# Optimization experiments

Hardware: AMD Instinct MI355X
Metric: run time of the kernel (lower is better)

## Reference

```python
import jax, jax.numpy as jnp
import numpy as np

B, S, D = 4, 2048, 1024
NH, NKV = 16, 4
HD = D // NH  # 64


def _rope(x, freqs):
    # x: [B, H, S, HD], freqs: [B, S, HD//2]
    cos = jnp.concatenate([jnp.cos(freqs), jnp.cos(freqs)], axis=-1)[:, None]  # [B,1,S,HD]
    sin = jnp.concatenate([jnp.sin(freqs), jnp.sin(freqs)], axis=-1)[:, None]
    x1, x2 = x[..., : HD // 2], x[..., HD // 2:]
    rot = jnp.concatenate([-x2, x1], axis=-1)
    return x * cos + rot * sin


def setup_inputs() -> dict:
    key = jax.random.key(0)
    ks = jax.random.split(key, 9)
    return {
        "hidden_states": jax.random.normal(ks[0], (B, S, D), jnp.float32),
        "rotary_pos_emb": jax.random.normal(ks[1], (B, S, HD // 2), jnp.float32),
        "Wq": jax.random.normal(ks[2], (D, NH * HD), jnp.float32) * 0.02,
        "bq": jax.random.normal(ks[3], (NH * HD,), jnp.float32) * 0.02,
        "Wk": jax.random.normal(ks[4], (D, NKV * HD), jnp.float32) * 0.02,
        "bk": jax.random.normal(ks[5], (NKV * HD,), jnp.float32) * 0.02,
        "Wv": jax.random.normal(ks[6], (D, NKV * HD), jnp.float32) * 0.02,
        "bv": jax.random.normal(ks[7], (NKV * HD,), jnp.float32) * 0.02,
        "Wo": jax.random.normal(ks[8], (NH * HD, D), jnp.float32) * 0.02,
    }


def reference(hidden_states, rotary_pos_emb, Wq, bq, Wk, bk, Wv, bv, Wo):
    b, s, _ = hidden_states.shape
    # projections -> [B, H, S, HD]
    q = (hidden_states @ Wq + bq).reshape(b, s, NH, HD).transpose(0, 2, 1, 3)
    k = (hidden_states @ Wk + bk).reshape(b, s, NKV, HD).transpose(0, 2, 1, 3)
    v = (hidden_states @ Wv + bv).reshape(b, s, NKV, HD).transpose(0, 2, 1, 3)
    q = _rope(q, rotary_pos_emb)
    k = _rope(k, rotary_pos_emb)
    groups = NH // NKV
    k = jnp.repeat(k, groups, axis=1)  # [B, NH, S, HD]
    v = jnp.repeat(v, groups, axis=1)
    scaling = HD ** -0.5
    scores = jnp.einsum("bhqd,bhkd->bhqk", q, k) * scaling
    probs = jax.nn.softmax(scores.astype(jnp.float32), axis=-1).astype(q.dtype)
    out = jnp.einsum("bhqk,bhkd->bhqd", probs, v)
    out = out.transpose(0, 2, 1, 3).reshape(b, s, NH * HD)
    return out @ Wo
```

## Files before the change

### kernel.cpp

```cpp
#include <hip/hip_runtime.h>
#include <hip/hip_bf16.h>

#define BB 4
#define SS 2048
#define DD 1024
#define NH 16
#define NKV 4
#define HD 64
#define MROWS (BB*SS)
#define NQKV (NH*HD + 2*NKV*HD)
#define KOFF (NH*HD)

typedef short v8s __attribute__((ext_vector_type(8)));
typedef short v4s __attribute__((ext_vector_type(4)));
typedef float v4f __attribute__((ext_vector_type(4)));
typedef unsigned short u16;
typedef unsigned int u32;

__device__ __forceinline__ float bf2f(u16 u){
  union { float f; u32 i; } x; x.i = ((u32)u) << 16; return x.f;
}
__device__ __forceinline__ u16 f2bf(float f){
  union { __hip_bfloat16 h; u16 u; } x; x.h = __float2bfloat16(f); return x.u;
}
__device__ __forceinline__ u32 cvtpk(float lo, float hi){
  u32 r;
  asm("v_cvt_pk_bf16_f32 %0, %1, %2" : "=v"(r) : "v"(lo), "v"(hi));
  return r;
}
__device__ __forceinline__ void gl_lds16(const u16* g, u16* l){
  __builtin_amdgcn_global_load_lds(
      (const __attribute__((address_space(1))) u32*)g,
      (__attribute__((address_space(3))) u32*)l, 16, 0, 0);
}


__global__ void prep_fused(const float* __restrict__ Wq, const float* __restrict__ Wk,
                           const float* __restrict__ Wv, const float* __restrict__ bq,
                           const float* __restrict__ bk, const float* __restrict__ bv,
                           const float* __restrict__ Wo, const float* __restrict__ fr,
                           u16* __restrict__ Bqkv, float* __restrict__ bias,
                           u16* __restrict__ WoT, float2* __restrict__ trig){
  int bid = blockIdx.x;
  if (bid < 6144) {
    int idx = bid*256 + threadIdx.x;
    int n = idx >> 10, k = idx & 1023;
    float v;
    if (n < 1024)      v = Wq[k*1024 + n];
    else if (n < 1280) v = Wk[k*256 + (n-1024)];
    else               v = Wv[k*256 + (n-1280)];
    Bqkv[idx] = f2bf(v);
    if (k == 0) bias[n] = (n < 1024) ? bq[n] : (n < 1280 ? bk[n-1024] : bv[n-1280]);
  } else if (bid < 6144 + 4096) {
    int idx = (bid - 6144)*256 + threadIdx.x;
    int n = idx >> 10, k = idx & 1023;
    WoT[idx] = f2bf(Wo[k*1024 + n]);
  } else {
    int i = (bid - 10240)*256 + threadIdx.x;
    float f = fr[i];
    float sn, cs; __sincosf(f, &sn, &cs);
    trig[i] = make_float2(cs, sn);
  }
}

__global__ void rope_k(u16* __restrict__ QKV, const float* __restrict__ fr){
  int idx = blockIdx.x*256 + threadIdx.x;
  int d  = idx & 31;
  int hh = (idx >> 5) & 3;
  long row = idx >> 7;
  int col = KOFF + hh*HD + d;
  u16* p = QKV + row*NQKV;
  float x1 = bf2f(p[col]);
  float x2 = bf2f(p[col+32]);
  float f = fr[row*32 + d];
  float sn, cs; __sincosf(f, &sn, &cs);
  p[col]    = f2bf(x1*cs - x2*sn);
  p[col+32] = f2bf(x2*cs + x1*sn);
}


template<bool BIAS, typename IT, typename OT>
__global__ __launch_bounds__(256) void gemm_bt(
    const IT* __restrict__ A, const u16* __restrict__ Bt,
    const float* __restrict__ bias, OT* __restrict__ C,
    int K, int ldc)
{
  __shared__ u16 As[128*32];
  __shared__ u16 Bs[128*32];
  const int tid = threadIdx.x;
  const int wid = tid >> 6, lane = tid & 63;
  const int g = lane >> 4, c = lane & 15;
  const long brow = (long)blockIdx.y * 128;
  const long bcol = (long)blockIdx.x * 128;
  const int wr = (wid >> 1) * 64, wc = (wid & 1) * 64;
  const int srow = tid >> 2;
  const int scol = (tid & 3) * 8;
  const IT*  ga = &A [(brow + srow)*K + scol];
  const u16* gb = &Bt[(bcol + srow)*K + scol];
  u16* la  = &As[(wid*64)*8];
  u16* lb  = &Bs[(wid*64)*8];
  u16* lwa = &As[srow*32 + scol];
  v4f acc[4][4] = {};
  for (int kt = 0; kt < K; kt += 32) {
    __syncthreads();
    gl_lds16(gb + kt,        lb);
    gl_lds16(gb + 64*K + kt, lb + 256*8);
    if constexpr (sizeof(IT) == 4) {
      float4 a0 = *reinterpret_cast<const float4*>(ga + kt);
      float4 a1 = *reinterpret_cast<const float4*>(ga + kt + 4);
      float4 a2 = *reinterpret_cast<const float4*>(ga + (long)64*K + kt);
      float4 a3 = *reinterpret_cast<const float4*>(ga + (long)64*K + kt + 4);
      union { v8s v; u32 w[4]; } p0, p1;
      p0.w[0] = cvtpk(a0.x, a0.y); p0.w[1] = cvtpk(a0.z, a0.w);
      p0.w[2] = cvtpk(a1.x, a1.y); p0.w[3] = cvtpk(a1.z, a1.w);
      p1.w[0] = cvtpk(a2.x, a2.y); p1.w[1] = cvtpk(a2.z, a2.w);
      p1.w[2] = cvtpk(a3.x, a3.y); p1.w[3] = cvtpk(a3.z, a3.w);
      *reinterpret_cast<v8s*>(lwa)          = p0.v;
      *reinterpret_cast<v8s*>(lwa + 64*32)  = p1.v;
    } else {
      gl_lds16((const u16*)ga + kt,        la);
      gl_lds16((const u16*)ga + 64*K + kt, la + 256*8);
    }
    __syncthreads();
    v8s af[4], bf[4];
    #pragma unroll
    for (int m=0;m<4;m++) af[m] = *reinterpret_cast<const v8s*>(&As[(wr + m*16 + c)*32 + g*8]);
    #pragma unroll
    for (int n=0;n<4;n++) bf[n] = *reinterpret_cast<const v8s*>(&Bs[(wc + n*16 + c)*32 + g*8]);
    __builtin_amdgcn_s_setprio(1);
    #pragma unroll
    for (int m=0;m<4;m++)
      #pragma unroll
      for (int n=0;n<4;n++)
        acc[m][n] = __builtin_amdgcn_mfma_f32_16x16x32_bf16(af[m], bf[n], acc[m][n], 0,0,0);
    __builtin_amdgcn_s_setprio(0);
  }
  #pragma unroll
  for (int m=0;m<4;m++)
    #pragma unroll
    for (int n=0;n<4;n++) {
      int col = (int)bcol + wc + n*16 + c;
      float badd = BIAS ? bias[col] : 0.0f;
      #pragma unroll
      for (int r2=0;r2<4;r2++){
        long row = brow + wr + m*16 + g*4 + r2;
        float v = acc[m][n][r2] + badd;
        if constexpr (sizeof(OT)==2) C[row*ldc + col] = (OT)f2bf(v);
        else                         C[row*ldc + col] = (OT)v;
      }
    }
}


__global__ __launch_bounds__(512) void attn_k(const u16* __restrict__ QKV,
                                              const float2* __restrict__ trig,
                                              u16* __restrict__ Out){
  __shared__ u16 Ks[4][64][72];
  __shared__ u16 Vs[4][64][72];
  const int tid = threadIdx.x;
  const int wid = tid >> 6, lane = tid & 63;
  const int g = lane >> 4, c = lane & 15;
  const int qt = blockIdx.x & 7;
  const int bh = blockIdx.x >> 3;
  const int b = bh >> 4, h = bh & 15;
  const int kvh = h >> 2;
  const u16* Qb = QKV + (long)b*SS*NQKV + h*HD;
  const u16* Kb = QKV + (long)b*SS*NQKV + KOFF + kvh*HD;
  const u16* Vb = Kb + NKV*HD;

  const float SCL = 0.125f * 1.44269504088896f;
  v8s qf[2][2];
  #pragma unroll
  for (int qn=0;qn<2;qn++){
    int lrow = qt*256 + wid*32 + qn*16 + c;
    v8s q0 = *reinterpret_cast<const v8s*>(&Qb[(long)lrow*NQKV + g*8]);
    v8s q1 = *reinterpret_cast<const v8s*>(&Qb[(long)lrow*NQKV + 32 + g*8]);
    const float2* tp = trig + ((long)b*SS + lrow)*32 + g*8;
    union { v8s v; u32 w[4]; } a0, a1;
    #pragma unroll
    for (int wi=0;wi<4;wi++){
      float2 ta = tp[2*wi], tb = tp[2*wi+1];
      float x1a = bf2f((u16)q0[2*wi]),   x2a = bf2f((u16)q1[2*wi]);
      float x1b = bf2f((u16)q0[2*wi+1]), x2b = bf2f((u16)q1[2*wi+1]);
      float r0a = (x1a*ta.x - x2a*ta.y) * SCL;
      float r1a = (x2a*ta.x + x1a*ta.y) * SCL;
      float r0b = (x1b*tb.x - x2b*tb.y) * SCL;
      float r1b = (x2b*tb.x + x1b*tb.y) * SCL;
      a0.w[wi] = cvtpk(r0a, r0b);
      a1.w[wi] = cvtpk(r1a, r1b);
    }
    qf[qn][0] = a0.v; qf[qn][1] = a1.v;
  }

  v8s onesf;
  {
    short ov = (c==0) ? (short)0x3F80 : (short)0;
    #pragma unroll
    for (int j=0;j<8;j++) onesf[j] = ov;
  }

  const v4f vzero = {0.f, 0.f, 0.f, 0.f};
  v4f o[2][5] = {};

  const int krow = tid >> 3;
  const int kcol = (tid & 7) * 8;
  const int key0 = 2*(tid >> 4);
  const int dg4  = (tid & 15) * 4;
  const int slot0 = 32*(key0>>5) + 8*((key0>>2)&3) + 4*((key0>>4)&1) + (key0&3);
  int vofs[4];
  #pragma unroll
  for (int j=0;j<4;j++){
    int d = dg4 + j;
    int idx = (((slot0>>3) ^ (d>>3)) << 3) | (slot0 & 7);
    vofs[j] = d*72 + idx;
  }
  u16* VsF = &Vs[0][0][0];

  const u16* kp  = Kb + (long)krow*NQKV + kcol;
  const u16* vp0 = Vb + (long)key0*NQKV + dg4;
  const u16* vp1 = vp0 + NQKV;

  v8s kregA, kregB;
  union { v4s v; u32 w[2]; } vrA0, vrA1, vrB0, vrB1;

  auto write_tile = [&](int q, const v8s& kr,
                        const u32* wA, const u32* wB){
    *reinterpret_cast<v8s*>(&Ks[q][krow][kcol]) = kr;
    const int bofs = q * (64*72);
    #pragma unroll
    for (int j=0;j<4;j++){
      u32 pkd = __builtin_amdgcn_perm(wB[j>>1], wA[j>>1],
                                      (j&1) ? 0x07060302u : 0x05040100u);
      *reinterpret_cast<u32*>(&VsF[bofs + vofs[j]]) = pkd;
    }
  };

  auto tile_body = [&](int buf){
    v8s kf0[4], kf1[4];
    #pragma unroll
    for (int km=0;km<4;km++){
      kf0[km] = *reinterpret_cast<const v8s*>(&Ks[buf][km*16 + c][g*8]);
      kf1[km] = *reinterpret_cast<const v8s*>(&Ks[buf][km*16 + c][32 + g*8]);
    }
    v4f st[4][2];
    __builtin_amdgcn_s_setprio(1);
    #pragma unroll
    for (int km=0;km<4;km++)
      #pragma unroll
      for (int qn=0;qn<2;qn++)
        st[km][qn] = __builtin_amdgcn_mfma_f32_16x16x32_bf16(kf0[km], qf[qn][0], vzero, 0,0,0);
    #pragma unroll
    for (int km=0;km<4;km++)
      #pragma unroll
      for (int qn=0;qn<2;qn++)
        st[km][qn] = __builtin_amdgcn_mfma_f32_16x16x32_bf16(kf1[km], qf[qn][1], st[km][qn], 0,0,0);
    __builtin_amdgcn_s_setprio(0);

    #pragma unroll
    for (int km=0;km<4;km++)
      #pragma unroll
      for (int qn=0;qn<2;qn++)
        #pragma unroll
        for (int r2=0;r2<4;r2++)
          st[km][qn][r2] = __builtin_amdgcn_exp2f(st[km][qn][r2]);

    v8s pa[2][2];
    #pragma unroll
    for (int qm=0;qm<2;qm++)
      #pragma unroll
      for (int ks=0;ks<2;ks++){
        union { v8s v; u32 w[4]; } u;
        u.w[0] = cvtpk(st[2*ks  ][qm][0], st[2*ks  ][qm][1]);
        u.w[1] = cvtpk(st[2*ks  ][qm][2], st[2*ks  ][qm][3]);
        u.w[2] = cvtpk(st[2*ks+1][qm][0], st[2*ks+1][qm][1]);
        u.w[3] = cvtpk(st[2*ks+1][qm][2], st[2*ks+1][qm][3]);
        pa[qm][ks] = u.v;
      }

    #pragma unroll
    for (int ks=0;ks<2;ks++){
      __builtin_amdgcn_s_setprio(1);
      #pragma unroll
      for (int dn=0;dn<4;dn++){
        int d0 = dn*16 + c;
        v8s vf = *reinterpret_cast<const v8s*>(&Vs[buf][d0][(((ks*4+g) ^ (d0>>3)) << 3)]);
        #pragma unroll
        for (int qm=0;qm<2;qm++)
          o[qm][dn] = __builtin_amdgcn_mfma_f32_16x16x32_bf16(pa[qm][ks], vf, o[qm][dn], 0,0,0);
      }
      #pragma unroll
      for (int qm=0;qm<2;qm++)
        o[qm][4] = __builtin_amdgcn_mfma_f32_16x16x32_bf16(pa[qm][ks], onesf, o[qm][4], 0,0,0);
      __builtin_amdgcn_s_setprio(0);
    }
  };

  {
    long off1 = (long)64*NQKV;
    kregA  = *reinterpret_cast<const v8s*>(kp);
    vrA0.v = *reinterpret_cast<const v4s*>(vp0);
    vrA1.v = *reinterpret_cast<const v4s*>(vp1);
    kregB  = *reinterpret_cast<const v8s*>(kp  + off1);
    vrB0.v = *reinterpret_cast<const v4s*>(vp0 + off1);
    vrB1.v = *reinterpret_cast<const v4s*>(vp1 + off1);
    write_tile(0, kregA, vrA0.w, vrA1.w);
    write_tile(1, kregB, vrB0.w, vrB1.w);
  }
  __syncthreads();

  for (int j = 0; j < SS/128; ++j){
    const int base = (j & 1) * 2;
    const bool pf = (j + 1 < SS/128);
    if (pf) {
      long offA = (long)(2*j+2)*64*NQKV;
      long offB = (long)(2*j+3)*64*NQKV;
      kregA  = *reinterpret_cast<const v8s*>(kp  + offA);
      vrA0.v = *reinterpret_cast<const v4s*>(vp0 + offA);
      vrA1.v = *reinterpret_cast<const v4s*>(vp1 + offA);
      kregB  = *reinterpret_cast<const v8s*>(kp  + offB);
      vrB0.v = *reinterpret_cast<const v4s*>(vp0 + offB);
      vrB1.v = *reinterpret_cast<const v4s*>(vp1 + offB);
    }

    tile_body(base);
    tile_body(base + 1);

    if (pf) {
      write_tile(base ^ 2,       kregA, vrA0.w, vrA1.w);
      write_tile((base ^ 2) + 1, kregB, vrB0.w, vrB1.w);
    }
    __syncthreads();
  }

  #pragma unroll
  for (int qm=0;qm<2;qm++)
    #pragma unroll
    for (int r2=0;r2<4;r2++){
      float l = __shfl(o[qm][4][r2], lane & 48);
      float inv = 1.0f / l;
      long row = (long)b*SS + qt*256 + wid*32 + qm*16 + g*4 + r2;
      #pragma unroll
      for (int dn=0;dn<4;dn++)
        Out[row*DD + h*HD + dn*16 + c] = f2bf(o[qm][dn][r2] * inv);
    }
}


extern "C" void kernel_launch(void* const* d_in, const int* in_sizes, int n_in,
                              void* d_out, int out_size, void* d_ws, size_t ws_size,
                              hipStream_t stream)
{
  const float* hs = (const float*)d_in[0];
  const float* fr = (const float*)d_in[1];
  const float* Wq = (const float*)d_in[2];
  const float* bq = (const float*)d_in[3];
  const float* Wk = (const float*)d_in[4];
  const float* bk = (const float*)d_in[5];
  const float* Wv = (const float*)d_in[6];
  const float* bv = (const float*)d_in[7];
  const float* Wo = (const float*)d_in[8];
  float* out = (float*)d_out;
  char* ws = (char*)d_ws;

  float2* trig = (float2*)ws;
  u16*   Bqkv = (u16*)(ws + 16777216);
  u16*   WoT  = (u16*)(ws + 16777216 + 3145728);
  float* bias = (float*)(ws + 16777216 + 3145728 + 2097152);
  u16*   QKV  = (u16*)(ws + 22028288);
  u16*   AO   = (u16*)(ws + 22028288 + 25165824);

  prep_fused<<<11264, 256, 0, stream>>>(Wq, Wk, Wv, bq, bk, bv, Wo, fr,
                                        Bqkv, bias, WoT, trig);
  gemm_bt<true,  float, u16> <<<dim3(NQKV/128, MROWS/128), 256, 0, stream>>>(hs, Bqkv, bias, QKV, DD, NQKV);
  rope_k    <<<MROWS*NKV*32/256, 256, 0, stream>>>(QKV, fr);
  attn_k    <<<BB*NH*(SS/256), 512, 0, stream>>>(QKV, trig, AO);
  gemm_bt<false, u16, float><<<dim3(DD/128, MROWS/128), 256, 0, stream>>>(AO, WoT, nullptr, out, DD, DD);
}
```

Before: 169.1 us.

## Fuse K RoPE into QKV GEMM epilogue and tile weight transposes

The separate rope_k kernel is removed. RoPE for the K heads is now applied in the QKV GEMM epilogue, using the precomputed cos/sin table, for warps whose 64-column slice covers a K head; this saves a launch and a read-modify-write pass over K. The weight-prep kernel now transposes through a 32x33 shared-memory tile so that both global reads and writes are coalesced, instead of the strided reads it did before. The epilogue for K tiles reads bias and trig per element, which adds some scattered loads there.

```diff
diff --git a/kernel.cpp b/kernel.cpp
--- a/kernel.cpp
+++ b/kernel.cpp
@@ -41,49 +41,50 @@
                            const float* __restrict__ Wo, const float* __restrict__ fr,
                            u16* __restrict__ Bqkv, float* __restrict__ bias,
                            u16* __restrict__ WoT, float2* __restrict__ trig){
-  int bid = blockIdx.x;
-  if (bid < 6144) {
-    int idx = bid*256 + threadIdx.x;
-    int n = idx >> 10, k = idx & 1023;
-    float v;
-    if (n < 1024)      v = Wq[k*1024 + n];
-    else if (n < 1280) v = Wk[k*256 + (n-1024)];
-    else               v = Wv[k*256 + (n-1280)];
-    Bqkv[idx] = f2bf(v);
-    if (k == 0) bias[n] = (n < 1024) ? bq[n] : (n < 1280 ? bk[n-1024] : bv[n-1280]);
-  } else if (bid < 6144 + 4096) {
-    int idx = (bid - 6144)*256 + threadIdx.x;
-    int n = idx >> 10, k = idx & 1023;
-    WoT[idx] = f2bf(Wo[k*1024 + n]);
+  __shared__ float T[32][33];
+  const int bid = blockIdx.x;
+  const int tid = threadIdx.x;
+  const int tx = tid & 31, ty = tid >> 5;
+  if (bid < 1536) {
+    const int kt = (bid & 31)*32, nt = (bid >> 5)*32;
+    const int n = nt + tx;
+    const float* src; int ld, nb;
+    if (nt < 1024)      { src = Wq; ld = 1024; nb = n; }
+    else if (nt < 1280) { src = Wk; ld = 256;  nb = n - 1024; }
+    else                { src = Wv; ld = 256;  nb = n - 1280; }
+    #pragma unroll
+    for (int i=0;i<4;i++)
+      T[ty + 8*i][tx] = src[(long)(kt + ty + 8*i)*ld + nb];
+    __syncthreads();
+    #pragma unroll
+    for (int i=0;i<4;i++)
+      Bqkv[(long)(nt + ty + 8*i)*1024 + kt + tx] = f2bf(T[tx][ty + 8*i]);
+    if ((bid & 31) == 0 && ty == 0)
+      bias[n] = (n < 1024) ? bq[n] : (n < 1280 ? bk[n-1024] : bv[n-1280]);
+  } else if (bid < 2560) {
+    const int b2 = bid - 1536;
+    const int kt = (b2 & 31)*32, nt = (b2 >> 5)*32;
+    #pragma unroll
+    for (int i=0;i<4;i++)
+      T[ty + 8*i][tx] = Wo[(long)(kt + ty + 8*i)*1024 + nt + tx];
+    __syncthreads();
+    #pragma unroll
+    for (int i=0;i<4;i++)
+      WoT[(long)(nt + ty + 8*i)*1024 + kt + tx] = f2bf(T[tx][ty + 8*i]);
   } else {
-    int i = (bid - 10240)*256 + threadIdx.x;
+    int i = (bid - 2560)*256 + tid;
     float f = fr[i];
     float sn, cs; __sincosf(f, &sn, &cs);
     trig[i] = make_float2(cs, sn);
   }
 }
 
-__global__ void rope_k(u16* __restrict__ QKV, const float* __restrict__ fr){
-  int idx = blockIdx.x*256 + threadIdx.x;
-  int d  = idx & 31;
-  int hh = (idx >> 5) & 3;
-  long row = idx >> 7;
-  int col = KOFF + hh*HD + d;
-  u16* p = QKV + row*NQKV;
-  float x1 = bf2f(p[col]);
-  float x2 = bf2f(p[col+32]);
-  float f = fr[row*32 + d];
-  float sn, cs; __sincosf(f, &sn, &cs);
-  p[col]    = f2bf(x1*cs - x2*sn);
-  p[col+32] = f2bf(x2*cs + x1*sn);
-}
-
 
 template<bool BIAS, typename IT, typename OT>
 __global__ __launch_bounds__(256) void gemm_bt(
     const IT* __restrict__ A, const u16* __restrict__ Bt,
-    const float* __restrict__ bias, OT* __restrict__ C,
-    int K, int ldc)
+    const float* __restrict__ bias, const float2* __restrict__ trig,
+    OT* __restrict__ C, int K, int ldc)
 {
   __shared__ u16 As[128*32];
   __shared__ u16 Bs[128*32];
@@ -135,20 +136,40 @@
         acc[m][n] = __builtin_amdgcn_mfma_f32_16x16x32_bf16(af[m], bf[n], acc[m][n], 0,0,0);
     __builtin_amdgcn_s_setprio(0);
   }
-  #pragma unroll
-  for (int m=0;m<4;m++)
-    #pragma unroll
-    for (int n=0;n<4;n++) {
-      int col = (int)bcol + wc + n*16 + c;
-      float badd = BIAS ? bias[col] : 0.0f;
+  const int cb = (int)bcol + wc;
+  if (BIAS && cb >= KOFF && cb < KOFF + NKV*HD) {
+    #pragma unroll
+    for (int m=0;m<4;m++)
       #pragma unroll
       for (int r2=0;r2<4;r2++){
         long row = brow + wr + m*16 + g*4 + r2;
-        float v = acc[m][n][r2] + badd;
-        if constexpr (sizeof(OT)==2) C[row*ldc + col] = (OT)f2bf(v);
-        else                         C[row*ldc + col] = (OT)v;
+        #pragma unroll
+        for (int np=0;np<2;np++){
+          int d = np*16 + c;
+          int col1 = cb + d, col2 = col1 + 32;
+          float v1 = acc[m][np  ][r2] + bias[col1];
+          float v2 = acc[m][np+2][r2] + bias[col2];
+          float2 t = trig[row*32 + d];
+          C[row*ldc + col1] = (OT)f2bf(v1*t.x - v2*t.y);
+          C[row*ldc + col2] = (OT)f2bf(v2*t.x + v1*t.y);
+        }
       }
-    }
+  } else {
+    #pragma unroll
+    for (int m=0;m<4;m++)
+      #pragma unroll
+      for (int n=0;n<4;n++) {
+        int col = cb + n*16 + c;
+        float badd = BIAS ? bias[col] : 0.0f;
+        #pragma unroll
+        for (int r2=0;r2<4;r2++){
+          long row = brow + wr + m*16 + g*4 + r2;
+          float v = acc[m][n][r2] + badd;
+          if constexpr (sizeof(OT)==2) C[row*ldc + col] = (OT)f2bf(v);
+          else                         C[row*ldc + col] = (OT)v;
+        }
+      }
+  }
 }
 
 
@@ -369,10 +390,9 @@
   u16*   QKV  = (u16*)(ws + 22028288);
   u16*   AO   = (u16*)(ws + 22028288 + 25165824);
 
-  prep_fused<<<11264, 256, 0, stream>>>(Wq, Wk, Wv, bq, bk, bv, Wo, fr,
-                                        Bqkv, bias, WoT, trig);
-  gemm_bt<true,  float, u16> <<<dim3(NQKV/128, MROWS/128), 256, 0, stream>>>(hs, Bqkv, bias, QKV, DD, NQKV);
-  rope_k    <<<MROWS*NKV*32/256, 256, 0, stream>>>(QKV, fr);
+  prep_fused<<<3584, 256, 0, stream>>>(Wq, Wk, Wv, bq, bk, bv, Wo, fr,
+                                       Bqkv, bias, WoT, trig);
+  gemm_bt<true,  float, u16> <<<dim3(NQKV/128, MROWS/128), 256, 0, stream>>>(hs, Bqkv, bias, trig, QKV, DD, NQKV);
   attn_k    <<<BB*NH*(SS/256), 512, 0, stream>>>(QKV, trig, AO);
-  gemm_bt<false, u16, float><<<dim3(DD/128, MROWS/128), 256, 0, stream>>>(AO, WoT, nullptr, out, DD, DD);
-}
+  gemm_bt<false, u16, float><<<dim3(DD/128, MROWS/128), 256, 0, stream>>>(AO, WoT, nullptr, nullptr, out, DD, DD);
+}
```

New measurement: 184.8 us. +9.3%, slower.
